# Kernel optimization log

Measured on AMD Instinct MI355X. Metric: run time of the kernel, lower is better.

Reference implementation:

```python
import jax, jax.numpy as jnp
import numpy as np

B, T, C = 2048, 64, 384  # batch, seq (== block_size), n_embd
HEAD = 64


def setup_inputs() -> dict:
    key = jax.random.key(0)
    k1, k2, k3, k4 = jax.random.split(key, 4)
    x = jax.random.normal(k1, (B, T, C), dtype=jnp.float32)
    Wq = jax.random.normal(k2, (C, HEAD), dtype=jnp.float32) * (C ** -0.5)
    Wk = jax.random.normal(k3, (C, HEAD), dtype=jnp.float32) * (C ** -0.5)
    Wv = jax.random.normal(k4, (C, HEAD), dtype=jnp.float32) * (C ** -0.5)
    return {"x": x, "Wq": Wq, "Wk": Wk, "Wv": Wv}


def reference(x, Wq, Wk, Wv):
    Bx, Tx, Cx = x.shape
    q = jnp.einsum('btc,ch->bth', x, Wq)
    k = jnp.einsum('btc,ch->bth', x, Wk)
    v = jnp.einsum('btc,ch->bth', x, Wv)
    # NOTE: original code scales by n_embd**-0.5 (C), not head_size**-0.5
    wei = jnp.einsum('bth,bsh->bts', q, k) * (Cx ** -0.5)
    causal = jnp.tril(jnp.ones((Tx, Tx), dtype=bool))  # tril[:T,:T]
    wei = jnp.where(causal, wei, -jnp.inf)
    wei = jax.nn.softmax(wei, axis=-1)
    # dropout is identity in eval mode
    out = jnp.einsum('bts,bsh->bth', wei, v)
    return out
```

## Files before the change

### kernel.cpp

```cpp
#include <hip/hip_runtime.h>
#include <stdint.h>

typedef _Float16 f16;
typedef _Float16 f16x8 __attribute__((ext_vector_type(8)));
typedef _Float16 f16x4 __attribute__((ext_vector_type(4)));
typedef float floatx4 __attribute__((ext_vector_type(4)));
typedef float floatx2 __attribute__((ext_vector_type(2)));

#define TT 64
#define CDIM 384
#define HH 64
#define NKK 12
#define LDP 72
#define OST 66
#define SCALE 0.05103103630798288f

__global__ void prep_w(const float* __restrict__ Wq,
                       const float* __restrict__ Wk,
                       const float* __restrict__ Wv,
                       f16* __restrict__ wf) {
    int t = blockIdx.x * 256 + threadIdx.x;
    if (t >= 3 * NKK * 4 * 64) return;
    int lane = t & 63;
    int tile = (t >> 6) & 3;
    int p    = (t >> 8) % 3;
    int kk   = t / 768;
    const float* W = (p == 0) ? Wq : ((p == 1) ? Wk : Wv);
    int n  = tile * 16 + (lane & 15);
    int k0 = kk * 32 + (lane >> 4) * 8;
    f16x8 frag;
#pragma unroll
    for (int j = 0; j < 8; ++j) frag[j] = (f16)W[(k0 + j) * HH + n];
    ((f16x8*)wf)[t] = frag;
}

__launch_bounds__(256, 4)
__global__ void attn_head(const float* __restrict__ x,
                          const f16* __restrict__ wf,
                          float* __restrict__ out) {
    __shared__ __align__(16) char smem[4 * TT * LDP * sizeof(f16)];
    f16* qs  = (f16*)smem;
    f16* ksm = qs  + TT * LDP;
    f16* vst = ksm + TT * LDP;
    f16* ps  = vst + TT * LDP;
    float* ost = (float*)smem;

    const int b    = blockIdx.x;
    const int tid  = threadIdx.x;
    const int wave = tid >> 6;
    const int lane = tid & 63;
    const int quad = lane >> 4;
    const int cl   = lane & 15;
    const int row0 = wave * 16;

    const floatx4 fzero = {0.f, 0.f, 0.f, 0.f};

    floatx4 acc[3][4];
#pragma unroll
    for (int p = 0; p < 3; ++p)
#pragma unroll
        for (int t = 0; t < 4; ++t) acc[p][t] = fzero;

    const float* xp = x + ((size_t)b * TT + row0 + cl) * CDIM + quad * 8;
    const f16x8* wg = (const f16x8*)wf;

#pragma unroll
    for (int kk = 0; kk < NKK; ++kk) {
        float4 f0 = *(const float4*)(xp + kk * 32);
        float4 f1 = *(const float4*)(xp + kk * 32 + 4);
        f16x8 xf;
        xf[0]=(f16)f0.x; xf[1]=(f16)f0.y; xf[2]=(f16)f0.z; xf[3]=(f16)f0.w;
        xf[4]=(f16)f1.x; xf[5]=(f16)f1.y; xf[6]=(f16)f1.z; xf[7]=(f16)f1.w;
        const f16x8* wk = wg + (size_t)kk * 768 + lane;
#pragma unroll
        for (int p = 0; p < 3; ++p)
#pragma unroll
            for (int t = 0; t < 4; ++t) {
                f16x8 bfrag = wk[(p * 4 + t) * 64];
                acc[p][t] = __builtin_amdgcn_mfma_f32_16x16x32_f16(
                    xf, bfrag, acc[p][t], 0, 0, 0);
            }
    }

#pragma unroll
    for (int t = 0; t < 4; ++t) {
        int h = t * 16 + cl;
#pragma unroll
        for (int r = 0; r < 4; ++r) {
            int tr = row0 + quad * 4 + r;
            qs [tr * LDP + h] = (f16)acc[0][t][r];
            ksm[tr * LDP + h] = (f16)acc[1][t][r];
        }
        f16x4 vv;
        vv[0]=(f16)acc[2][t][0]; vv[1]=(f16)acc[2][t][1];
        vv[2]=(f16)acc[2][t][2]; vv[3]=(f16)acc[2][t][3];
        *(f16x4*)&vst[h * LDP + row0 + quad * 4] = vv;
    }
    __syncthreads();

    floatx4 sa[4];
#pragma unroll
    for (int t = 0; t < 4; ++t) sa[t] = fzero;
#pragma unroll
    for (int kv = 0; kv < 2; ++kv) {
        f16x8 aq = *(const f16x8*)&qs[(row0 + cl) * LDP + kv * 32 + quad * 8];
#pragma unroll
        for (int t = 0; t < 4; ++t) {
            f16x8 bk = *(const f16x8*)&ksm[(t * 16 + cl) * LDP + kv * 32 + quad * 8];
            sa[t] = __builtin_amdgcn_mfma_f32_16x16x32_f16(aq, bk, sa[t], 0, 0, 0);
        }
    }

#pragma unroll
    for (int r = 0; r < 4; ++r) {
        int tr = row0 + quad * 4 + r;
        float v0[4];
        float m = -1e30f;
#pragma unroll
        for (int t = 0; t < 4; ++t) {
            int s = t * 16 + cl;
            float v = sa[t][r] * SCALE;
            v = (s <= tr) ? v : -1e30f;
            v0[t] = v;
            m = fmaxf(m, v);
        }
#pragma unroll
        for (int off = 1; off < 16; off <<= 1) m = fmaxf(m, __shfl_xor(m, off));
        float sum = 0.f;
#pragma unroll
        for (int t = 0; t < 4; ++t) { v0[t] = __expf(v0[t] - m); sum += v0[t]; }
#pragma unroll
        for (int off = 1; off < 16; off <<= 1) sum += __shfl_xor(sum, off);
        float inv = 1.0f / sum;
#pragma unroll
        for (int t = 0; t < 4; ++t)
            ps[tr * LDP + t * 16 + cl] = (f16)(v0[t] * inv);
    }
    __syncthreads();

    floatx4 oa[4];
#pragma unroll
    for (int t = 0; t < 4; ++t) oa[t] = fzero;
#pragma unroll
    for (int kv = 0; kv < 2; ++kv) {
        f16x8 ap = *(const f16x8*)&ps[(row0 + cl) * LDP + kv * 32 + quad * 8];
#pragma unroll
        for (int t = 0; t < 4; ++t) {
            f16x8 bv = *(const f16x8*)&vst[(t * 16 + cl) * LDP + kv * 32 + quad * 8];
            oa[t] = __builtin_amdgcn_mfma_f32_16x16x32_f16(ap, bv, oa[t], 0, 0, 0);
        }
    }

#pragma unroll
    for (int t = 0; t < 4; ++t)
#pragma unroll
        for (int r = 0; r < 4; ++r)
            ost[(row0 + quad * 4 + r) * OST + t * 16 + cl] = oa[t][r];
    __syncthreads();

    float* op = out + (size_t)b * TT * HH;
#pragma unroll
    for (int i = 0; i < 4; ++i) {
        int row = i * 16 + (tid >> 4);
        int c4  = (tid & 15) * 4;
        floatx2 lo = *(const floatx2*)&ost[row * OST + c4];
        floatx2 hi = *(const floatx2*)&ost[row * OST + c4 + 2];
        float4 v; v.x = lo[0]; v.y = lo[1]; v.z = hi[0]; v.w = hi[1];
        *(float4*)&op[row * HH + c4] = v;
    }
}

extern "C" void kernel_launch(void* const* d_in, const int* in_sizes, int n_in,
                              void* d_out, int out_size, void* d_ws, size_t ws_size,
                              hipStream_t stream) {
    const float* x  = (const float*)d_in[0];
    const float* Wq = (const float*)d_in[1];
    const float* Wk = (const float*)d_in[2];
    const float* Wv = (const float*)d_in[3];
    float* out = (float*)d_out;
    f16* wf = (f16*)d_ws;

    prep_w<<<36, 256, 0, stream>>>(Wq, Wk, Wv, wf);
    attn_head<<<2048, 256, 0, stream>>>(x, wf, out);
}
```

Measured before the change: 321.4 us.

## Stage x in LDS and split QKV projection by output tiles across waves

The QKV projection is restructured so the block's x tile is converted to fp16 and staged in shared memory in two halves, and each wave computes 3 of the 12 output column tiles for all 64 rows. Before, each wave covered 16 rows and reloaded all 12 weight fragments per k-step. Now each wave loads only its own 3 weight fragments per k-step, which cuts global and L2 weight traffic by about four times. The global loads for the second half of x are issued before the first-half MFMAs so they overlap. The cost is extra LDS round-trips and __syncthreads barriers, plus more live registers (hreg), which may lower occupancy.

```diff
diff --git a/kernel.cpp b/kernel.cpp
--- a/kernel.cpp
+++ b/kernel.cpp
@@ -11,6 +11,7 @@
 #define CDIM 384
 #define HH 64
 #define NKK 12
+#define KH 6
 #define LDP 72
 #define OST 66
 #define SCALE 0.05103103630798288f
@@ -34,11 +35,19 @@
     ((f16x8*)wf)[t] = frag;
 }
 
+static __device__ __forceinline__ f16x8 cvt8(float4 f0, float4 f1) {
+    f16x8 h;
+    h[0]=(f16)f0.x; h[1]=(f16)f0.y; h[2]=(f16)f0.z; h[3]=(f16)f0.w;
+    h[4]=(f16)f1.x; h[5]=(f16)f1.y; h[6]=(f16)f1.z; h[7]=(f16)f1.w;
+    return h;
+}
+
 __launch_bounds__(256, 4)
 __global__ void attn_head(const float* __restrict__ x,
                           const f16* __restrict__ wf,
                           float* __restrict__ out) {
     __shared__ __align__(16) char smem[4 * TT * LDP * sizeof(f16)];
+    f16* stg = (f16*)smem;
     f16* qs  = (f16*)smem;
     f16* ksm = qs  + TT * LDP;
     f16* vst = ksm + TT * LDP;
@@ -53,48 +62,94 @@
     const int cl   = lane & 15;
     const int row0 = wave * 16;
 
+    const int r_st = tid >> 2;
+    const int qd   = tid & 3;
+    const int l_st = qd * 16 + (r_st & 15);
+    const int mt_st = r_st >> 4;
+    const float* xr = x + ((size_t)b * TT + r_st) * CDIM + qd * 8;
+
     const floatx4 fzero = {0.f, 0.f, 0.f, 0.f};
-
     floatx4 acc[3][4];
 #pragma unroll
-    for (int p = 0; p < 3; ++p)
-#pragma unroll
-        for (int t = 0; t < 4; ++t) acc[p][t] = fzero;
-
-    const float* xp = x + ((size_t)b * TT + row0 + cl) * CDIM + quad * 8;
+    for (int j = 0; j < 3; ++j)
+#pragma unroll
+        for (int mt = 0; mt < 4; ++mt) acc[j][mt] = fzero;
+
     const f16x8* wg = (const f16x8*)wf;
 
-#pragma unroll
-    for (int kk = 0; kk < NKK; ++kk) {
-        float4 f0 = *(const float4*)(xp + kk * 32);
-        float4 f1 = *(const float4*)(xp + kk * 32 + 4);
-        f16x8 xf;
-        xf[0]=(f16)f0.x; xf[1]=(f16)f0.y; xf[2]=(f16)f0.z; xf[3]=(f16)f0.w;
-        xf[4]=(f16)f1.x; xf[5]=(f16)f1.y; xf[6]=(f16)f1.z; xf[7]=(f16)f1.w;
-        const f16x8* wk = wg + (size_t)kk * 768 + lane;
-#pragma unroll
-        for (int p = 0; p < 3; ++p)
-#pragma unroll
-            for (int t = 0; t < 4; ++t) {
-                f16x8 bfrag = wk[(p * 4 + t) * 64];
-                acc[p][t] = __builtin_amdgcn_mfma_f32_16x16x32_f16(
-                    xf, bfrag, acc[p][t], 0, 0, 0);
+    f16x8 hreg[KH];
+#pragma unroll
+    for (int i = 0; i < KH; ++i)
+        hreg[i] = cvt8(*(const float4*)(xr + i * 32),
+                       *(const float4*)(xr + i * 32 + 4));
+#pragma unroll
+    for (int i = 0; i < KH; ++i)
+        *(f16x8*)&stg[((i * 4 + mt_st) * 64 + l_st) * 8] = hreg[i];
+    __syncthreads();
+
+#pragma unroll
+    for (int i = 0; i < KH; ++i)
+        hreg[i] = cvt8(*(const float4*)(xr + (KH + i) * 32),
+                       *(const float4*)(xr + (KH + i) * 32 + 4));
+
+#pragma unroll
+    for (int i = 0; i < KH; ++i) {
+        f16x8 af[4];
+#pragma unroll
+        for (int mt = 0; mt < 4; ++mt)
+            af[mt] = *(const f16x8*)&stg[((i * 4 + mt) * 64 + lane) * 8];
+#pragma unroll
+        for (int j = 0; j < 3; ++j) {
+            f16x8 bf = wg[(size_t)i * 768 + (wave * 3 + j) * 64 + lane];
+#pragma unroll
+            for (int mt = 0; mt < 4; ++mt)
+                acc[j][mt] = __builtin_amdgcn_mfma_f32_16x16x32_f16(
+                    af[mt], bf, acc[j][mt], 0, 0, 0);
+        }
+    }
+    __syncthreads();
+#pragma unroll
+    for (int i = 0; i < KH; ++i)
+        *(f16x8*)&stg[((i * 4 + mt_st) * 64 + l_st) * 8] = hreg[i];
+    __syncthreads();
+#pragma unroll
+    for (int i = 0; i < KH; ++i) {
+        f16x8 af[4];
+#pragma unroll
+        for (int mt = 0; mt < 4; ++mt)
+            af[mt] = *(const f16x8*)&stg[((i * 4 + mt) * 64 + lane) * 8];
+#pragma unroll
+        for (int j = 0; j < 3; ++j) {
+            f16x8 bf = wg[(size_t)(KH + i) * 768 + (wave * 3 + j) * 64 + lane];
+#pragma unroll
+            for (int mt = 0; mt < 4; ++mt)
+                acc[j][mt] = __builtin_amdgcn_mfma_f32_16x16x32_f16(
+                    af[mt], bf, acc[j][mt], 0, 0, 0);
+        }
+    }
+    __syncthreads();
+
+#pragma unroll
+    for (int j = 0; j < 3; ++j) {
+        int T  = wave * 3 + j;
+        int p  = T >> 2;
+        int h  = (T & 3) * 16 + cl;
+        if (p == 2) {
+#pragma unroll
+            for (int mt = 0; mt < 4; ++mt) {
+                f16x4 vv;
+                vv[0]=(f16)acc[j][mt][0]; vv[1]=(f16)acc[j][mt][1];
+                vv[2]=(f16)acc[j][mt][2]; vv[3]=(f16)acc[j][mt][3];
+                *(f16x4*)&vst[h * LDP + mt * 16 + quad * 4] = vv;
             }
-    }
-
-#pragma unroll
-    for (int t = 0; t < 4; ++t) {
-        int h = t * 16 + cl;
-#pragma unroll
-        for (int r = 0; r < 4; ++r) {
-            int tr = row0 + quad * 4 + r;
-            qs [tr * LDP + h] = (f16)acc[0][t][r];
-            ksm[tr * LDP + h] = (f16)acc[1][t][r];
-        }
-        f16x4 vv;
-        vv[0]=(f16)acc[2][t][0]; vv[1]=(f16)acc[2][t][1];
-        vv[2]=(f16)acc[2][t][2]; vv[3]=(f16)acc[2][t][3];
-        *(f16x4*)&vst[h * LDP + row0 + quad * 4] = vv;
+        } else {
+            f16* dst = (p == 0) ? qs : ksm;
+#pragma unroll
+            for (int mt = 0; mt < 4; ++mt)
+#pragma unroll
+                for (int r = 0; r < 4; ++r)
+                    dst[(mt * 16 + quad * 4 + r) * LDP + h] = (f16)acc[j][mt][r];
+        }
     }
     __syncthreads();
 
```

Result: faster. 299.3 us (-6.9%).

## Stage projection weights in LDS via async global_load_lds double buffering

Applied to the files above, without the earlier changes.

Each wave used to read its weight fragments for the QKV projection directly from global memory, one load per MFMA. Now the block loads each 32-wide K chunk of the packed weights into LDS with global_load_lds, double-buffered so the next chunk arrives while the current one is consumed. It also loads the x fragment one step ahead. The goal is to cut redundant global weight traffic across the four waves and hide load latency. The cost is a __syncthreads per K step and LDS reads for the B fragments.

```diff
diff --git a/kernel.cpp b/kernel.cpp
--- a/kernel.cpp
+++ b/kernel.cpp
@@ -13,6 +13,7 @@
 #define NKK 12
 #define LDP 72
 #define OST 66
+#define CHUNK 12288
 #define SCALE 0.05103103630798288f
 
 __global__ void prep_w(const float* __restrict__ Wq,
@@ -34,15 +35,29 @@
     ((f16x8*)wf)[t] = frag;
 }
 
+static __device__ __forceinline__ f16x8 cvt8(float4 f0, float4 f1) {
+    f16x8 h;
+    h[0]=(f16)f0.x; h[1]=(f16)f0.y; h[2]=(f16)f0.z; h[3]=(f16)f0.w;
+    h[4]=(f16)f1.x; h[5]=(f16)f1.y; h[6]=(f16)f1.z; h[7]=(f16)f1.w;
+    return h;
+}
+
+static __device__ __forceinline__ void glds16(const void* g, void* l) {
+    __builtin_amdgcn_global_load_lds(
+        (const __attribute__((address_space(1))) uint32_t*)g,
+        (__attribute__((address_space(3))) uint32_t*)l, 16, 0, 0);
+}
+
 __launch_bounds__(256, 4)
 __global__ void attn_head(const float* __restrict__ x,
                           const f16* __restrict__ wf,
                           float* __restrict__ out) {
     __shared__ __align__(16) char smem[4 * TT * LDP * sizeof(f16)];
-    f16* qs  = (f16*)smem;
-    f16* ksm = qs  + TT * LDP;
-    f16* vst = ksm + TT * LDP;
-    f16* ps  = vst + TT * LDP;
+    f16* wbuf = (f16*)smem;
+    f16* qs   = (f16*)smem;
+    f16* ksm  = qs  + TT * LDP;
+    f16* vst  = ksm + TT * LDP;
+    f16* ps   = vst + TT * LDP;
     float* ost = (float*)smem;
 
     const int b    = blockIdx.x;
@@ -54,47 +69,60 @@
     const int row0 = wave * 16;
 
     const floatx4 fzero = {0.f, 0.f, 0.f, 0.f};
-
-    floatx4 acc[3][4];
-#pragma unroll
-    for (int p = 0; p < 3; ++p)
-#pragma unroll
-        for (int t = 0; t < 4; ++t) acc[p][t] = fzero;
+    floatx4 acc[12];
+#pragma unroll
+    for (int T = 0; T < 12; ++T) acc[T] = fzero;
 
     const float* xp = x + ((size_t)b * TT + row0 + cl) * CDIM + quad * 8;
-    const f16x8* wg = (const f16x8*)wf;
-
-#pragma unroll
+    const char* wb  = (const char*)wf;
+    const int lslot = (wave * 64 + lane) * 16;
+
+    float4 xa = *(const float4*)(xp);
+    float4 xb = *(const float4*)(xp + 4);
+
+#pragma unroll
+    for (int j = 0; j < 3; ++j)
+        glds16(wb + j * 4096 + lslot, wbuf + j * 2048 + wave * 512);
+
+#pragma unroll 2
     for (int kk = 0; kk < NKK; ++kk) {
-        float4 f0 = *(const float4*)(xp + kk * 32);
-        float4 f1 = *(const float4*)(xp + kk * 32 + 4);
-        f16x8 xf;
-        xf[0]=(f16)f0.x; xf[1]=(f16)f0.y; xf[2]=(f16)f0.z; xf[3]=(f16)f0.w;
-        xf[4]=(f16)f1.x; xf[5]=(f16)f1.y; xf[6]=(f16)f1.z; xf[7]=(f16)f1.w;
-        const f16x8* wk = wg + (size_t)kk * 768 + lane;
-#pragma unroll
-        for (int p = 0; p < 3; ++p)
-#pragma unroll
-            for (int t = 0; t < 4; ++t) {
-                f16x8 bfrag = wk[(p * 4 + t) * 64];
-                acc[p][t] = __builtin_amdgcn_mfma_f32_16x16x32_f16(
-                    xf, bfrag, acc[p][t], 0, 0, 0);
-            }
-    }
-
-#pragma unroll
-    for (int t = 0; t < 4; ++t) {
-        int h = t * 16 + cl;
-#pragma unroll
-        for (int r = 0; r < 4; ++r) {
-            int tr = row0 + quad * 4 + r;
-            qs [tr * LDP + h] = (f16)acc[0][t][r];
-            ksm[tr * LDP + h] = (f16)acc[1][t][r];
-        }
-        f16x4 vv;
-        vv[0]=(f16)acc[2][t][0]; vv[1]=(f16)acc[2][t][1];
-        vv[2]=(f16)acc[2][t][2]; vv[3]=(f16)acc[2][t][3];
-        *(f16x4*)&vst[h * LDP + row0 + quad * 4] = vv;
+        __syncthreads();
+        const int cur = kk & 1;
+        if (kk + 1 < NKK) {
+#pragma unroll
+            for (int j = 0; j < 3; ++j)
+                glds16(wb + (kk + 1) * CHUNK + j * 4096 + lslot,
+                       wbuf + (1 - cur) * (CHUNK / 2) + j * 2048 + wave * 512);
+        }
+        f16x8 xf = cvt8(xa, xb);
+        if (kk + 1 < NKK) {
+            xa = *(const float4*)(xp + (kk + 1) * 32);
+            xb = *(const float4*)(xp + (kk + 1) * 32 + 4);
+        }
+        const f16* wc = wbuf + cur * (CHUNK / 2);
+#pragma unroll
+        for (int T = 0; T < 12; ++T) {
+            f16x8 bf = *(const f16x8*)&wc[(T * 64 + lane) * 8];
+            acc[T] = __builtin_amdgcn_mfma_f32_16x16x32_f16(xf, bf, acc[T], 0, 0, 0);
+        }
+    }
+    __syncthreads();
+
+#pragma unroll
+    for (int T = 0; T < 12; ++T) {
+        int p = T >> 2;
+        int h = (T & 3) * 16 + cl;
+        if (p == 2) {
+            f16x4 vv;
+            vv[0]=(f16)acc[T][0]; vv[1]=(f16)acc[T][1];
+            vv[2]=(f16)acc[T][2]; vv[3]=(f16)acc[T][3];
+            *(f16x4*)&vst[h * LDP + row0 + quad * 4] = vv;
+        } else {
+            f16* dst = p ? ksm : qs;
+#pragma unroll
+            for (int r = 0; r < 4; ++r)
+                dst[(row0 + quad * 4 + r) * LDP + h] = (f16)acc[T][r];
+        }
     }
     __syncthreads();
 
```

After: 299.9 us. 1.07x faster.
